# Kernel tuning notes

Hardware: AMD Instinct MI355X
Metric: run time of the kernel (lower is better)

The kernel has to match this reference:

```python
import jax, jax.numpy as jnp
import numpy as np

B, S, D = 32, 512, 512
H, DK, DV, DFF = 8, 64, 64, 2048
TEMP = float(np.sqrt(DK))  # d_k ** 0.5
COS_EPS = 1e-8             # torch.cosine_similarity eps
LN_EPS = 1e-5


def _layernorm(x, g, b):
    mu = jnp.mean(x, axis=-1, keepdims=True)
    var = jnp.var(x, axis=-1, keepdims=True)
    return (x - mu) * jax.lax.rsqrt(var + LN_EPS) * g + b


def setup_inputs() -> dict:
    key = jax.random.key(0)
    ks = jax.random.split(key, 12)
    s = 0.02
    return {
        "x": jax.random.normal(ks[0], (B, S, D), dtype=jnp.float32),
        "w_q": jax.random.normal(ks[1], (D, H * DK), dtype=jnp.float32) * s,
        "w_k": jax.random.normal(ks[2], (D, H * DK), dtype=jnp.float32) * s,
        "w_v": jax.random.normal(ks[3], (D, H * DV), dtype=jnp.float32) * s,
        "w_o": jax.random.normal(ks[4], (H * DV, D), dtype=jnp.float32) * s,
        "w_ff1": jax.random.normal(ks[5], (D, DFF), dtype=jnp.float32) * s,
        "b_ff1": jnp.zeros((DFF,), dtype=jnp.float32),
        "w_ff2": jax.random.normal(ks[6], (DFF, D), dtype=jnp.float32) * s,
        "b_ff2": jnp.zeros((D,), dtype=jnp.float32),
        "g1": jnp.ones((D,), dtype=jnp.float32),
        "b1": jnp.zeros((D,), dtype=jnp.float32),
        "g2": jnp.ones((D,), dtype=jnp.float32),
        "b2": jnp.zeros((D,), dtype=jnp.float32),
    }


def reference(x, w_q, w_k, w_v, w_o, w_ff1, b_ff1, w_ff2, b_ff2, g1, b1, g2, b2):
    b, s, _ = x.shape
    # projections -> [b, h, s, d]
    q = (x @ w_q).reshape(b, s, H, DK).transpose(0, 2, 1, 3)
    k = (x @ w_k).reshape(b, s, H, DK).transpose(0, 2, 1, 3)
    v = (x @ w_v).reshape(b, s, H, DV).transpose(0, 2, 1, 3)
    # cosine-similarity attention: dot(q,k) / max(||q||*||k||, eps) / temperature
    scores = jnp.einsum("bhqd,bhkd->bhqk", q, k)
    nq = jnp.linalg.norm(q, axis=-1)  # [b,h,s]
    nk = jnp.linalg.norm(k, axis=-1)
    denom = jnp.maximum(nq[:, :, :, None] * nk[:, :, None, :], COS_EPS)
    attn = jax.nn.softmax(scores / denom / TEMP, axis=-1)
    out = jnp.einsum("bhqk,bhkd->bhqd", attn, v)  # [b,h,s,dv]
    out = out.transpose(0, 2, 1, 3).reshape(b, s, H * DV) @ w_o
    # residual + LN1
    h1 = _layernorm(x + out, g1, b1)
    # FFN
    ffn = jax.nn.relu(h1 @ w_ff1 + b_ff1) @ w_ff2 + b_ff2
    # residual + LN2
    return _layernorm(h1 + ffn, g2, b2)
```

## Files before the change

### kernel.cpp

```cpp
#include <hip/hip_runtime.h>
#include <cmath>

typedef __bf16 bf16x8 __attribute__((ext_vector_type(8)));
typedef float  floatx4 __attribute__((ext_vector_type(4)));

#define LN_EPS 1e-5f
#define COS_EPS 1e-8f
#define INV_TEMP 0.125f

static const int Mrows = 16384;

__device__ __forceinline__ void gload_lds16(const void* g, void* l) {
  __builtin_amdgcn_global_load_lds(
      (const __attribute__((address_space(1))) void*)g,
      (__attribute__((address_space(3))) void*)l, 16, 0, 0);
}

__global__ __launch_bounds__(256) void prep_kernel(const float* __restrict__ x, __bf16* __restrict__ xb,
                                                   const float* __restrict__ wq, const float* __restrict__ wk,
                                                   const float* __restrict__ wv, const float* __restrict__ wo,
                                                   const float* __restrict__ wff1, const float* __restrict__ wff2,
                                                   __bf16* __restrict__ tq, __bf16* __restrict__ tk,
                                                   __bf16* __restrict__ tv, __bf16* __restrict__ to_,
                                                   __bf16* __restrict__ tff1, __bf16* __restrict__ tff2) {
  const int bid = blockIdx.x, tid = threadIdx.x;
  if (bid < 8192) {
    int i = bid * 256 + tid;
    float4 v = ((const float4*)x)[i];
    __bf16* d = xb + i * 4;
    d[0] = (__bf16)v.x; d[1] = (__bf16)v.y; d[2] = (__bf16)v.z; d[3] = (__bf16)v.w;
    return;
  }
  __shared__ __bf16 til[64][72];
  int t = bid - 8192;
  const float* src; __bf16* dst; int R, C, bx, by;
  if (t < 256) {
    int w = t >> 6, tt = t & 63;
    const float* srcs[4] = {wq, wk, wv, wo};
    __bf16* dsts[4] = {tq, tk, tv, to_};
    src = srcs[w]; dst = dsts[w]; R = 512; C = 512; bx = tt & 7; by = tt >> 3;
  } else if (t < 512) {
    int tt = t - 256;
    src = wff1; dst = tff1; R = 512; C = 2048; bx = tt & 31; by = tt >> 5;
  } else {
    int tt = t - 512;
    src = wff2; dst = tff2; R = 2048; C = 512; bx = tt & 7; by = tt >> 3;
  }
  const float* s = src + (size_t)(by * 64) * C + bx * 64;
  int r = tid >> 4, c4 = (tid & 15) * 4;
  for (int p = 0; p < 4; ++p) {
    int rr = r + p * 16;
    float4 v = *(const float4*)(s + (size_t)rr * C + c4);
    til[c4 + 0][rr] = (__bf16)v.x;
    til[c4 + 1][rr] = (__bf16)v.y;
    til[c4 + 2][rr] = (__bf16)v.z;
    til[c4 + 3][rr] = (__bf16)v.w;
  }
  __syncthreads();
  __bf16* d = dst + (size_t)(bx * 64) * R + by * 64;
  int orow = tid >> 3, oc8 = (tid & 7) * 8;
  for (int p = 0; p < 2; ++p) {
    int rr = orow + p * 32;
    *(bf16x8*)(d + (size_t)rr * R + oc8) = *(const bf16x8*)(&til[rr][oc8]);
  }
}

template <int EPI>
__global__ __launch_bounds__(256) void gemm_bt(const __bf16* __restrict__ A,
                                               const __bf16* __restrict__ Bt,
                                               __bf16* __restrict__ Cv,
                                               const float* __restrict__ bias,
                                               float* __restrict__ norms,
                                               int nbn, int Ndim, int Kdim) {
  __shared__ __align__(16) char smem[128 * 144 * 2];
  __bf16* As = (__bf16*)smem;
  __bf16* Bs = (__bf16*)(smem + 32768 / 2);
  const int tid = threadIdx.x;
  const int wave = tid >> 6, lane = tid & 63;
  const int l15 = lane & 15, quad = lane >> 4;
  const int id = blockIdx.x;
  const int xcd = id & 7, t = id >> 3;
  const int nblk = t % nbn, mblk = (t / nbn) * 8 + xcd;
  const int m0 = mblk * 128, n0 = nblk * 128;
  const int wrow = (wave >> 1) * 64, wcol = (wave & 1) * 64;
  const int rs = lane >> 3;
  const int swz_st = ((lane & 7) ^ rs) * 8;
  const int s7 = l15 & 7;

  floatx4 zero = {0.f, 0.f, 0.f, 0.f};
  floatx4 acc[4][4];
  for (int i = 0; i < 4; ++i)
    for (int j = 0; j < 4; ++j) acc[i][j] = zero;

  for (int kt = 0; kt < Kdim; kt += 64) {
    __syncthreads();
    for (int c = 0; c < 8; ++c) {
      int g = wave * 8 + c;
      const __bf16* src;
      __bf16* dst;
      if (g < 16) {
        int row = m0 + g * 8 + rs;
        src = A + (size_t)row * Kdim + kt + swz_st;
        dst = As + g * 512;
      } else {
        int g2 = g - 16;
        int row = n0 + g2 * 8 + rs;
        src = Bt + (size_t)row * Kdim + kt + swz_st;
        dst = Bs + g2 * 512;
      }
      gload_lds16(src, dst + lane * 8);
    }
    __syncthreads();
    for (int hh = 0; hh < 2; ++hh) {
      int ko = ((hh * 4 + quad) ^ s7) * 8;
      bf16x8 a[4], b[4];
      for (int i = 0; i < 4; ++i)
        a[i] = *(const bf16x8*)(As + (wrow + i * 16 + l15) * 64 + ko);
      for (int j = 0; j < 4; ++j)
        b[j] = *(const bf16x8*)(Bs + (wcol + j * 16 + l15) * 64 + ko);
      for (int i = 0; i < 4; ++i)
        for (int j = 0; j < 4; ++j)
          acc[i][j] = __builtin_amdgcn_mfma_f32_16x16x32_bf16(a[i], b[j], acc[i][j], 0, 0, 0);
    }
  }

  if (EPI == 4) {
    int head_global = (n0 + wcol) >> 6;
    int kind = head_global >> 3;
    if (kind < 2) {
      int h = head_global & 7;
      for (int i = 0; i < 4; ++i)
        for (int r = 0; r < 4; ++r) {
          float sq = 0.f;
          for (int j = 0; j < 4; ++j) {
            float v = acc[i][j][r];
            sq += v * v;
          }
          for (int m = 1; m < 16; m <<= 1) sq += __shfl_xor(sq, m, 64);
          if (l15 == 0) {
            int arow = m0 + wrow + i * 16 + quad * 4 + r;
            int bb = arow >> 9, ss = arow & 511;
            norms[kind * 131072 + ((bb << 3) + h) * 512 + ss] = sqrtf(sq);
          }
        }
    }
  }

  __syncthreads();
  __bf16* Cs = (__bf16*)smem;
  for (int i = 0; i < 4; ++i)
    for (int j = 0; j < 4; ++j) {
      int coll = wcol + j * 16 + l15;
      float bv = (EPI == 2) ? bias[n0 + coll] : 0.f;
      for (int r = 0; r < 4; ++r) {
        float v = acc[i][j][r];
        if (EPI == 2) {
          v += bv;
          v = v > 0.f ? v : 0.f;
        }
        Cs[(wrow + i * 16 + quad * 4 + r) * 144 + coll] = (__bf16)v;
      }
    }
  __syncthreads();
  for (int p = 0; p < 8; ++p) {
    int row = p * 16 + (tid >> 4);
    int c8 = (tid & 15) * 8;
    *(bf16x8*)(Cv + (size_t)(m0 + row) * Ndim + n0 + c8) =
        *(const bf16x8*)(Cs + row * 144 + c8);
  }
}

__global__ __launch_bounds__(256) void vtrans_kernel(const __bf16* __restrict__ qkv,
                                                     __bf16* __restrict__ vtg) {
  __shared__ __align__(16) unsigned short til[64][68];
  const int tid = threadIdx.x;
  const int st = blockIdx.x;
  const int bh = blockIdx.y;
  const int b = bh >> 3, h = bh & 7;
  const unsigned short* src = (const unsigned short*)qkv +
      (size_t)(b * 512 + st * 64) * 1536 + 1024 + h * 64;
  for (int it = 0; it < 2; ++it) {
    int row = it * 32 + (tid >> 3);
    int c8 = (tid & 7) * 8;
    bf16x8 v = *(const bf16x8*)((const __bf16*)src + (size_t)row * 1536 + c8);
    for (int i = 0; i < 8; ++i) til[row][c8 + i] = ((unsigned short*)&v)[i];
  }
  __syncthreads();
  unsigned short* dst = (unsigned short*)vtg + (size_t)bh * 32768 + st * 64;
  for (int it = 0; it < 2; ++it) {
    int d = it * 32 + (tid >> 3);
    int s8 = (tid & 7) * 8;
    unsigned short v[8];
    for (int i = 0; i < 8; ++i) v[i] = til[s8 + i][d];
    *(bf16x8*)(dst + (size_t)d * 512 + s8) = *(bf16x8*)v;
  }
}

__global__ __launch_bounds__(256) void attn_kernel(const __bf16* __restrict__ qkv,
                                                   const __bf16* __restrict__ vtg,
                                                   const float* __restrict__ norms,
                                                   __bf16* __restrict__ out) {
  __shared__ __align__(16) __bf16 Ks[64 * 64];
  __shared__ __align__(16) __bf16 Vs[64 * 64];
  __shared__ __align__(16) __bf16 P[4][16 * 72];
  const int tid = threadIdx.x, wave = tid >> 6, lane = tid & 63;
  const int l15 = lane & 15, quad = lane >> 4;
  const int bh = blockIdx.x & 255;
  const int qh = blockIdx.x >> 8;
  const int b = bh >> 3, h = bh & 7;
  const int qbase = qh * 256 + wave * 64;
  const int rs = lane >> 3;
  const int swz_st = ((lane & 7) ^ rs) * 8;
  const int s7 = l15 & 7;

  const __bf16* Qb = qkv + (size_t)(b * 512) * 1536 + h * 64;
  const __bf16* Kb = Qb + 512;
  const __bf16* Vtb = vtg + (size_t)bh * 32768;
  const float* nkbase = norms + 131072 + bh * 512;
  __bf16* Pw = P[wave];

  bf16x8 aq[4][2];
  float nq[4][4];
  for (int ch = 0; ch < 4; ++ch) {
    int qrow = qbase + ch * 16;
    aq[ch][0] = *(const bf16x8*)(Qb + (size_t)(qrow + l15) * 1536 + quad * 8);
    aq[ch][1] = *(const bf16x8*)(Qb + (size_t)(qrow + l15) * 1536 + 32 + quad * 8);
    for (int r = 0; r < 4; ++r) nq[ch][r] = norms[bh * 512 + qrow + quad * 4 + r];
  }

  floatx4 zero = {0.f, 0.f, 0.f, 0.f};
  floatx4 o[4][4];
  float lsum[4][4];
  for (int ch = 0; ch < 4; ++ch)
    for (int jd = 0; jd < 4; ++jd) o[ch][jd] = zero;
  for (int ch = 0; ch < 4; ++ch)
    for (int r = 0; r < 4; ++r) lsum[ch][r] = 0.f;

  for (int kt = 0; kt < 8; ++kt) {
    int s0 = kt * 64;
    __syncthreads();
    for (int c = 0; c < 4; ++c) {
      int g = wave * 4 + c;
      const __bf16* src;
      __bf16* dst;
      if (g < 8) {
        int sk = g * 8 + rs;
        src = Kb + (size_t)(s0 + sk) * 1536 + swz_st;
        dst = Ks + g * 512;
      } else {
        int g2 = g - 8;
        int d = g2 * 8 + rs;
        src = Vtb + (size_t)d * 512 + s0 + swz_st;
        dst = Vs + g2 * 512;
      }
      gload_lds16(src, dst + lane * 8);
    }
    __syncthreads();

    float nk[4];
    for (int j = 0; j < 4; ++j) nk[j] = nkbase[s0 + j * 16 + l15];

    for (int ch = 0; ch < 4; ++ch) {
      floatx4 z[4];
      for (int j = 0; j < 4; ++j) {
        int r64 = (j * 16 + l15) * 64;
        bf16x8 b0 = *(const bf16x8*)(Ks + r64 + ((quad ^ s7) * 8));
        bf16x8 b1 = *(const bf16x8*)(Ks + r64 + (((4 + quad) ^ s7) * 8));
        floatx4 zz = zero;
        zz = __builtin_amdgcn_mfma_f32_16x16x32_bf16(aq[ch][0], b0, zz, 0, 0, 0);
        zz = __builtin_amdgcn_mfma_f32_16x16x32_bf16(aq[ch][1], b1, zz, 0, 0, 0);
        z[j] = zz;
      }
      for (int j = 0; j < 4; ++j)
        for (int r = 0; r < 4; ++r) {
          float den = nq[ch][r] * nk[j];
          den = den > COS_EPS ? den : COS_EPS;
          float p = __expf(z[j][r] * __builtin_amdgcn_rcpf(den) * INV_TEMP);
          lsum[ch][r] += p;
          Pw[(quad * 4 + r) * 72 + j * 16 + l15] = (__bf16)p;
        }
      bf16x8 ap0 = *(const bf16x8*)(Pw + l15 * 72 + quad * 8);
      bf16x8 ap1 = *(const bf16x8*)(Pw + l15 * 72 + 32 + quad * 8);
      for (int jd = 0; jd < 4; ++jd) {
        int r64 = (jd * 16 + l15) * 64;
        bf16x8 v0 = *(const bf16x8*)(Vs + r64 + ((quad ^ s7) * 8));
        bf16x8 v1 = *(const bf16x8*)(Vs + r64 + (((4 + quad) ^ s7) * 8));
        o[ch][jd] = __builtin_amdgcn_mfma_f32_16x16x32_bf16(ap0, v0, o[ch][jd], 0, 0, 0);
        o[ch][jd] = __builtin_amdgcn_mfma_f32_16x16x32_bf16(ap1, v1, o[ch][jd], 0, 0, 0);
      }
    }
  }

  for (int ch = 0; ch < 4; ++ch)
    for (int r = 0; r < 4; ++r) {
      float s = lsum[ch][r];
      for (int m = 1; m < 16; m <<= 1) s += __shfl_xor(s, m, 64);
      lsum[ch][r] = __builtin_amdgcn_rcpf(s);
    }
  for (int ch = 0; ch < 4; ++ch)
    for (int jd = 0; jd < 4; ++jd)
      for (int r = 0; r < 4; ++r) {
        int q = qbase + ch * 16 + quad * 4 + r;
        int d = jd * 16 + l15;
        out[(size_t)(b * 512 + q) * 512 + h * 64 + d] = (__bf16)(o[ch][jd][r] * lsum[ch][r]);
      }
}

template <bool X1BF, bool WF, bool WB>
__global__ __launch_bounds__(256) void resid_ln(const float* __restrict__ X1f,
                                                const __bf16* __restrict__ X1b,
                                                const __bf16* __restrict__ X2,
                                                const float* __restrict__ bias,
                                                const float* __restrict__ g,
                                                const float* __restrict__ be,
                                                float* __restrict__ outf,
                                                __bf16* __restrict__ outb) {
  int row = blockIdx.x * 4 + (threadIdx.x >> 6);
  int lane = threadIdx.x & 63;
  float v[8];
  bf16x8 b8 = *(const bf16x8*)(X2 + (size_t)row * 512 + lane * 8);
  if (X1BF) {
    bf16x8 a = *(const bf16x8*)(X1b + (size_t)row * 512 + lane * 8);
    for (int i = 0; i < 8; ++i) v[i] = (float)a[i] + (float)b8[i];
  } else {
    const float4* r1 = (const float4*)(X1f + (size_t)row * 512);
    float4 a0 = r1[lane * 2], a1 = r1[lane * 2 + 1];
    v[0] = a0.x; v[1] = a0.y; v[2] = a0.z; v[3] = a0.w;
    v[4] = a1.x; v[5] = a1.y; v[6] = a1.z; v[7] = a1.w;
    for (int i = 0; i < 8; ++i) v[i] += (float)b8[i];
  }
  if (bias) {
    const float* bp = bias + lane * 8;
    for (int i = 0; i < 8; ++i) v[i] += bp[i];
  }
  float s = 0.f, sq = 0.f;
  for (int i = 0; i < 8; ++i) {
    s += v[i];
    sq += v[i] * v[i];
  }
  for (int m = 1; m < 64; m <<= 1) {
    s += __shfl_xor(s, m, 64);
    sq += __shfl_xor(sq, m, 64);
  }
  float mean = s * (1.f / 512.f);
  float var = sq * (1.f / 512.f) - mean * mean;
  float rstd = rsqrtf(var + LN_EPS);
  const float* gp = g + lane * 8;
  const float* bp2 = be + lane * 8;
  float o[8];
  for (int i = 0; i < 8; ++i) o[i] = (v[i] - mean) * rstd * gp[i] + bp2[i];
  if (WF) {
    float4 w0 = {o[0], o[1], o[2], o[3]}, w1 = {o[4], o[5], o[6], o[7]};
    ((float4*)(outf + (size_t)row * 512))[lane * 2] = w0;
    ((float4*)(outf + (size_t)row * 512))[lane * 2 + 1] = w1;
  }
  if (WB) {
    __bf16 tmp[8];
    for (int i = 0; i < 8; ++i) tmp[i] = (__bf16)o[i];
    *(bf16x8*)(outb + (size_t)row * 512 + lane * 8) = *(bf16x8*)tmp;
  }
}

extern "C" void kernel_launch(void* const* d_in, const int* in_sizes, int n_in,
                              void* d_out, int out_size, void* d_ws, size_t ws_size,
                              hipStream_t stream) {
  const float* x     = (const float*)d_in[0];
  const float* w_q   = (const float*)d_in[1];
  const float* w_k   = (const float*)d_in[2];
  const float* w_v   = (const float*)d_in[3];
  const float* w_o   = (const float*)d_in[4];
  const float* w_ff1 = (const float*)d_in[5];
  const float* b_ff1 = (const float*)d_in[6];
  const float* w_ff2 = (const float*)d_in[7];
  const float* b_ff2 = (const float*)d_in[8];
  const float* g1    = (const float*)d_in[9];
  const float* b1    = (const float*)d_in[10];
  const float* g2    = (const float*)d_in[11];
  const float* b2    = (const float*)d_in[12];
  float* out = (float*)d_out;

  char* ws = (char*)d_ws;
  size_t off = 0;
  auto alloc = [&](size_t bytes) -> void* {
    void* p = ws + off;
    off += (bytes + 255) & ~(size_t)255;
    return p;
  };
  __bf16* xb     = (__bf16*)alloc((size_t)Mrows * 512 * 2);
  __bf16* wt_qkv = (__bf16*)alloc((size_t)1536 * 512 * 2);
  __bf16* wt_o   = (__bf16*)alloc((size_t)512 * 512 * 2);
  __bf16* wt_ff1 = (__bf16*)alloc((size_t)2048 * 512 * 2);
  __bf16* wt_ff2 = (__bf16*)alloc((size_t)512 * 2048 * 2);
  __bf16* qkv    = (__bf16*)alloc((size_t)Mrows * 1536 * 2);
  float*  norms  = (float*)alloc((size_t)262144 * 4);
  __bf16* attn   = (__bf16*)alloc((size_t)Mrows * 512 * 2);
  __bf16* projb  = (__bf16*)alloc((size_t)Mrows * 512 * 2);
  __bf16* h1b    = (__bf16*)alloc((size_t)Mrows * 512 * 2);
  __bf16* mid    = (__bf16*)alloc((size_t)Mrows * 2048 * 2);
  __bf16* vtg    = mid;
  __bf16* f2o    = attn;

  prep_kernel<<<8960, 256, 0, stream>>>(x, xb, w_q, w_k, w_v, w_o, w_ff1, w_ff2,
                                        wt_qkv, wt_qkv + 512 * 512, wt_qkv + 2 * 512 * 512,
                                        wt_o, wt_ff1, wt_ff2);

  gemm_bt<4><<<dim3(12 * 128), 256, 0, stream>>>(xb, wt_qkv, qkv, nullptr,
                                                 norms, 12, 1536, 512);
  vtrans_kernel<<<dim3(8, 256), 256, 0, stream>>>(qkv, vtg);
  attn_kernel<<<dim3(512), 256, 0, stream>>>(qkv, vtg, norms, attn);
  gemm_bt<0><<<dim3(4 * 128), 256, 0, stream>>>(attn, wt_o, projb, nullptr,
                                                nullptr, 4, 512, 512);
  resid_ln<false, false, true><<<4096, 256, 0, stream>>>(x, nullptr, projb, nullptr,
                                                         g1, b1, nullptr, h1b);
  gemm_bt<2><<<dim3(16 * 128), 256, 0, stream>>>(h1b, wt_ff1, mid, b_ff1,
                                                 nullptr, 16, 2048, 512);
  gemm_bt<0><<<dim3(4 * 128), 256, 0, stream>>>(mid, wt_ff2, f2o, nullptr,
                                                nullptr, 4, 512, 2048);
  resid_ln<true, true, false><<<4096, 256, 0, stream>>>(nullptr, h1b, f2o, b_ff2,
                                                        g2, b2, out, nullptr);
}
```

Before: 339.7 us.

## Fuse V transpose into QKV GEMM epilogue and restructure attention with inverse norms

The QKV GEMM epilogue now writes V tiles transposed straight into the per-head V^T buffer, which removes the separate vtrans kernel and its extra pass over V. Q and K norms are stored as reciprocals, so attention multiplies instead of clamping and dividing; this drops the COS_EPS clamp and gives inf if a norm is zero. Attention swaps MFMA operand order so each lane owns a query row, which allows vectorised P and output stores and a cheaper row-sum reduction. It also halves queries per block to launch twice as many blocks. GEMM dimensions become template constants.

```diff
diff --git a/kernel.cpp b/kernel.cpp
--- a/kernel.cpp
+++ b/kernel.cpp
@@ -2,10 +2,10 @@
 #include <cmath>
 
 typedef __bf16 bf16x8 __attribute__((ext_vector_type(8)));
+typedef __bf16 bf16x4 __attribute__((ext_vector_type(4)));
 typedef float  floatx4 __attribute__((ext_vector_type(4)));
 
 #define LN_EPS 1e-5f
-#define COS_EPS 1e-8f
 #define INV_TEMP 0.125f
 
 static const int Mrows = 16384;
@@ -65,22 +65,22 @@
   }
 }
 
-template <int EPI>
+template <int EPI, int NBN, int NDIM, int KDIM>
 __global__ __launch_bounds__(256) void gemm_bt(const __bf16* __restrict__ A,
                                                const __bf16* __restrict__ Bt,
                                                __bf16* __restrict__ Cv,
                                                const float* __restrict__ bias,
                                                float* __restrict__ norms,
-                                               int nbn, int Ndim, int Kdim) {
+                                               __bf16* __restrict__ vtg) {
   __shared__ __align__(16) char smem[128 * 144 * 2];
   __bf16* As = (__bf16*)smem;
-  __bf16* Bs = (__bf16*)(smem + 32768 / 2);
+  __bf16* Bs = (__bf16*)(smem + 16384);
   const int tid = threadIdx.x;
   const int wave = tid >> 6, lane = tid & 63;
   const int l15 = lane & 15, quad = lane >> 4;
   const int id = blockIdx.x;
   const int xcd = id & 7, t = id >> 3;
-  const int nblk = t % nbn, mblk = (t / nbn) * 8 + xcd;
+  const int nblk = t % NBN, mblk = (t / NBN) * 8 + xcd;
   const int m0 = mblk * 128, n0 = nblk * 128;
   const int wrow = (wave >> 1) * 64, wcol = (wave & 1) * 64;
   const int rs = lane >> 3;
@@ -92,7 +92,7 @@
   for (int i = 0; i < 4; ++i)
     for (int j = 0; j < 4; ++j) acc[i][j] = zero;
 
-  for (int kt = 0; kt < Kdim; kt += 64) {
+  for (int kt = 0; kt < KDIM; kt += 64) {
     __syncthreads();
     for (int c = 0; c < 8; ++c) {
       int g = wave * 8 + c;
@@ -100,12 +100,12 @@
       __bf16* dst;
       if (g < 16) {
         int row = m0 + g * 8 + rs;
-        src = A + (size_t)row * Kdim + kt + swz_st;
+        src = A + (size_t)row * KDIM + kt + swz_st;
         dst = As + g * 512;
       } else {
         int g2 = g - 16;
         int row = n0 + g2 * 8 + rs;
-        src = Bt + (size_t)row * Kdim + kt + swz_st;
+        src = Bt + (size_t)row * KDIM + kt + swz_st;
         dst = Bs + g2 * 512;
       }
       gload_lds16(src, dst + lane * 8);
@@ -140,9 +140,29 @@
           if (l15 == 0) {
             int arow = m0 + wrow + i * 16 + quad * 4 + r;
             int bb = arow >> 9, ss = arow & 511;
-            norms[kind * 131072 + ((bb << 3) + h) * 512 + ss] = sqrtf(sq);
+            norms[kind * 131072 + ((bb << 3) + h) * 512 + ss] = rsqrtf(sq);
           }
         }
+    } else {
+      __syncthreads();
+      __bf16* Ct = (__bf16*)smem;
+      for (int i = 0; i < 4; ++i)
+        for (int j = 0; j < 4; ++j) {
+          bf16x4 pk;
+          for (int r = 0; r < 4; ++r) pk[r] = (__bf16)acc[i][j][r];
+          *(bf16x4*)(Ct + (wcol + j * 16 + l15) * 136 + wrow + i * 16 + quad * 4) = pk;
+        }
+      __syncthreads();
+      int b = mblk >> 2, s0r = (mblk & 3) * 128;
+      for (int p = 0; p < 8; ++p) {
+        int row = p * 16 + (tid >> 4);
+        int c8 = (tid & 15) * 8;
+        int colg = n0 + row;
+        int h = (colg >> 6) & 7, d = colg & 63;
+        *(bf16x8*)(vtg + ((size_t)(((b << 3) + h) * 64 + d)) * 512 + s0r + c8) =
+            *(const bf16x8*)(Ct + row * 136 + c8);
+      }
+      return;
     }
   }
 
@@ -165,34 +185,8 @@
   for (int p = 0; p < 8; ++p) {
     int row = p * 16 + (tid >> 4);
     int c8 = (tid & 15) * 8;
-    *(bf16x8*)(Cv + (size_t)(m0 + row) * Ndim + n0 + c8) =
+    *(bf16x8*)(Cv + (size_t)(m0 + row) * NDIM + n0 + c8) =
         *(const bf16x8*)(Cs + row * 144 + c8);
-  }
-}
-
-__global__ __launch_bounds__(256) void vtrans_kernel(const __bf16* __restrict__ qkv,
-                                                     __bf16* __restrict__ vtg) {
-  __shared__ __align__(16) unsigned short til[64][68];
-  const int tid = threadIdx.x;
-  const int st = blockIdx.x;
-  const int bh = blockIdx.y;
-  const int b = bh >> 3, h = bh & 7;
-  const unsigned short* src = (const unsigned short*)qkv +
-      (size_t)(b * 512 + st * 64) * 1536 + 1024 + h * 64;
-  for (int it = 0; it < 2; ++it) {
-    int row = it * 32 + (tid >> 3);
-    int c8 = (tid & 7) * 8;
-    bf16x8 v = *(const bf16x8*)((const __bf16*)src + (size_t)row * 1536 + c8);
-    for (int i = 0; i < 8; ++i) til[row][c8 + i] = ((unsigned short*)&v)[i];
-  }
-  __syncthreads();
-  unsigned short* dst = (unsigned short*)vtg + (size_t)bh * 32768 + st * 64;
-  for (int it = 0; it < 2; ++it) {
-    int d = it * 32 + (tid >> 3);
-    int s8 = (tid & 7) * 8;
-    unsigned short v[8];
-    for (int i = 0; i < 8; ++i) v[i] = til[s8 + i][d];
-    *(bf16x8*)(dst + (size_t)d * 512 + s8) = *(bf16x8*)v;
   }
 }
 
@@ -202,13 +196,13 @@
                                                    __bf16* __restrict__ out) {
   __shared__ __align__(16) __bf16 Ks[64 * 64];
   __shared__ __align__(16) __bf16 Vs[64 * 64];
-  __shared__ __align__(16) __bf16 P[4][16 * 72];
+  __shared__ __align__(16) __bf16 P2[4][16 * 72];
   const int tid = threadIdx.x, wave = tid >> 6, lane = tid & 63;
   const int l15 = lane & 15, quad = lane >> 4;
   const int bh = blockIdx.x & 255;
-  const int qh = blockIdx.x >> 8;
+  const int qq = blockIdx.x >> 8;
   const int b = bh >> 3, h = bh & 7;
-  const int qbase = qh * 256 + wave * 64;
+  const int qbase = qq * 128 + wave * 32;
   const int rs = lane >> 3;
   const int swz_st = ((lane & 7) ^ rs) * 8;
   const int s7 = l15 & 7;
@@ -216,25 +210,24 @@
   const __bf16* Qb = qkv + (size_t)(b * 512) * 1536 + h * 64;
   const __bf16* Kb = Qb + 512;
   const __bf16* Vtb = vtg + (size_t)bh * 32768;
-  const float* nkbase = norms + 131072 + bh * 512;
-  __bf16* Pw = P[wave];
-
-  bf16x8 aq[4][2];
-  float nq[4][4];
-  for (int ch = 0; ch < 4; ++ch) {
+  const float* nkinv = norms + 131072 + bh * 512;
+  const float* nqinv = norms + bh * 512;
+  __bf16* Pw = P2[wave];
+
+  bf16x8 aq[2][2];
+  float cq[2];
+  for (int ch = 0; ch < 2; ++ch) {
     int qrow = qbase + ch * 16;
     aq[ch][0] = *(const bf16x8*)(Qb + (size_t)(qrow + l15) * 1536 + quad * 8);
     aq[ch][1] = *(const bf16x8*)(Qb + (size_t)(qrow + l15) * 1536 + 32 + quad * 8);
-    for (int r = 0; r < 4; ++r) nq[ch][r] = norms[bh * 512 + qrow + quad * 4 + r];
+    cq[ch] = nqinv[qrow + l15] * INV_TEMP;
   }
 
   floatx4 zero = {0.f, 0.f, 0.f, 0.f};
-  floatx4 o[4][4];
-  float lsum[4][4];
-  for (int ch = 0; ch < 4; ++ch)
+  floatx4 o[2][4];
+  float lsum[2] = {0.f, 0.f};
+  for (int ch = 0; ch < 2; ++ch)
     for (int jd = 0; jd < 4; ++jd) o[ch][jd] = zero;
-  for (int ch = 0; ch < 4; ++ch)
-    for (int r = 0; r < 4; ++r) lsum[ch][r] = 0.f;
 
   for (int kt = 0; kt < 8; ++kt) {
     int s0 = kt * 64;
@@ -257,53 +250,52 @@
     }
     __syncthreads();
 
-    float nk[4];
-    for (int j = 0; j < 4; ++j) nk[j] = nkbase[s0 + j * 16 + l15];
-
-    for (int ch = 0; ch < 4; ++ch) {
+    for (int ch = 0; ch < 2; ++ch) {
       floatx4 z[4];
       for (int j = 0; j < 4; ++j) {
         int r64 = (j * 16 + l15) * 64;
-        bf16x8 b0 = *(const bf16x8*)(Ks + r64 + ((quad ^ s7) * 8));
-        bf16x8 b1 = *(const bf16x8*)(Ks + r64 + (((4 + quad) ^ s7) * 8));
+        bf16x8 k0 = *(const bf16x8*)(Ks + r64 + ((quad ^ s7) * 8));
+        bf16x8 k1 = *(const bf16x8*)(Ks + r64 + (((4 + quad) ^ s7) * 8));
         floatx4 zz = zero;
-        zz = __builtin_amdgcn_mfma_f32_16x16x32_bf16(aq[ch][0], b0, zz, 0, 0, 0);
-        zz = __builtin_amdgcn_mfma_f32_16x16x32_bf16(aq[ch][1], b1, zz, 0, 0, 0);
+        zz = __builtin_amdgcn_mfma_f32_16x16x32_bf16(k0, aq[ch][0], zz, 0, 0, 0);
+        zz = __builtin_amdgcn_mfma_f32_16x16x32_bf16(k1, aq[ch][1], zz, 0, 0, 0);
         z[j] = zz;
       }
-      for (int j = 0; j < 4; ++j)
+      for (int j = 0; j < 4; ++j) {
+        floatx4 nk4 = *(const floatx4*)(nkinv + s0 + j * 16 + quad * 4);
+        bf16x4 pk;
         for (int r = 0; r < 4; ++r) {
-          float den = nq[ch][r] * nk[j];
-          den = den > COS_EPS ? den : COS_EPS;
-          float p = __expf(z[j][r] * __builtin_amdgcn_rcpf(den) * INV_TEMP);
-          lsum[ch][r] += p;
-          Pw[(quad * 4 + r) * 72 + j * 16 + l15] = (__bf16)p;
+          float p = __expf(z[j][r] * cq[ch] * nk4[r]);
+          lsum[ch] += p;
+          pk[r] = (__bf16)p;
         }
+        *(bf16x4*)(Pw + l15 * 72 + j * 16 + quad * 4) = pk;
+      }
       bf16x8 ap0 = *(const bf16x8*)(Pw + l15 * 72 + quad * 8);
       bf16x8 ap1 = *(const bf16x8*)(Pw + l15 * 72 + 32 + quad * 8);
       for (int jd = 0; jd < 4; ++jd) {
         int r64 = (jd * 16 + l15) * 64;
         bf16x8 v0 = *(const bf16x8*)(Vs + r64 + ((quad ^ s7) * 8));
         bf16x8 v1 = *(const bf16x8*)(Vs + r64 + (((4 + quad) ^ s7) * 8));
-        o[ch][jd] = __builtin_amdgcn_mfma_f32_16x16x32_bf16(ap0, v0, o[ch][jd], 0, 0, 0);
-        o[ch][jd] = __builtin_amdgcn_mfma_f32_16x16x32_bf16(ap1, v1, o[ch][jd], 0, 0, 0);
-      }
-    }
-  }
-
-  for (int ch = 0; ch < 4; ++ch)
-    for (int r = 0; r < 4; ++r) {
-      float s = lsum[ch][r];
-      for (int m = 1; m < 16; m <<= 1) s += __shfl_xor(s, m, 64);
-      lsum[ch][r] = __builtin_amdgcn_rcpf(s);
-    }
-  for (int ch = 0; ch < 4; ++ch)
-    for (int jd = 0; jd < 4; ++jd)
-      for (int r = 0; r < 4; ++r) {
-        int q = qbase + ch * 16 + quad * 4 + r;
-        int d = jd * 16 + l15;
-        out[(size_t)(b * 512 + q) * 512 + h * 64 + d] = (__bf16)(o[ch][jd][r] * lsum[ch][r]);
-      }
+        o[ch][jd] = __builtin_amdgcn_mfma_f32_16x16x32_bf16(v0, ap0, o[ch][jd], 0, 0, 0);
+        o[ch][jd] = __builtin_amdgcn_mfma_f32_16x16x32_bf16(v1, ap1, o[ch][jd], 0, 0, 0);
+      }
+    }
+  }
+
+  for (int ch = 0; ch < 2; ++ch) {
+    float s = lsum[ch];
+    s += __shfl_xor(s, 16, 64);
+    s += __shfl_xor(s, 32, 64);
+    float inv = __builtin_amdgcn_rcpf(s);
+    int q = qbase + ch * 16 + l15;
+    __bf16* op = out + (size_t)(b * 512 + q) * 512 + h * 64;
+    for (int jd = 0; jd < 4; ++jd) {
+      bf16x4 pk;
+      for (int r = 0; r < 4; ++r) pk[r] = (__bf16)(o[ch][jd][r] * inv);
+      *(bf16x4*)(op + jd * 16 + quad * 4) = pk;
+    }
+  }
 }
 
 template <bool X1BF, bool WF, bool WB>
@@ -404,18 +396,17 @@
                                         wt_qkv, wt_qkv + 512 * 512, wt_qkv + 2 * 512 * 512,
                                         wt_o, wt_ff1, wt_ff2);
 
-  gemm_bt<4><<<dim3(12 * 128), 256, 0, stream>>>(xb, wt_qkv, qkv, nullptr,
-                                                 norms, 12, 1536, 512);
-  vtrans_kernel<<<dim3(8, 256), 256, 0, stream>>>(qkv, vtg);
-  attn_kernel<<<dim3(512), 256, 0, stream>>>(qkv, vtg, norms, attn);
-  gemm_bt<0><<<dim3(4 * 128), 256, 0, stream>>>(attn, wt_o, projb, nullptr,
-                                                nullptr, 4, 512, 512);
+  gemm_bt<4, 12, 1536, 512><<<dim3(12 * 128), 256, 0, stream>>>(xb, wt_qkv, qkv, nullptr,
+                                                                norms, vtg);
+  attn_kernel<<<dim3(1024), 256, 0, stream>>>(qkv, vtg, norms, attn);
+  gemm_bt<0, 4, 512, 512><<<dim3(4 * 128), 256, 0, stream>>>(attn, wt_o, projb, nullptr,
+                                                             nullptr, nullptr);
   resid_ln<false, false, true><<<4096, 256, 0, stream>>>(x, nullptr, projb, nullptr,
                                                          g1, b1, nullptr, h1b);
-  gemm_bt<2><<<dim3(16 * 128), 256, 0, stream>>>(h1b, wt_ff1, mid, b_ff1,
-                                                 nullptr, 16, 2048, 512);
-  gemm_bt<0><<<dim3(4 * 128), 256, 0, stream>>>(mid, wt_ff2, f2o, nullptr,
-                                                nullptr, 4, 512, 2048);
+  gemm_bt<2, 16, 2048, 512><<<dim3(16 * 128), 256, 0, stream>>>(h1b, wt_ff1, mid, b_ff1,
+                                                                nullptr, nullptr);
+  gemm_bt<0, 4, 512, 2048><<<dim3(4 * 128), 256, 0, stream>>>(mid, wt_ff2, f2o, nullptr,
+                                                              nullptr, nullptr);
   resid_ln<true, true, false><<<4096, 256, 0, stream>>>(nullptr, h1b, f2o, b_ff2,
                                                         g2, b2, out, nullptr);
 }
```

Result: faster. 328.2 us (-3.4%).
